# Kernel optimization log

Measured on AMD Instinct MI355X. Metric: run time of the kernel, lower is better.

The kernel has to match this reference:

```python
import jax, jax.numpy as jnp
import numpy as np

B, Himg, Wimg, C, NH = 16, 64, 64, 256, 8
HD = C // NH  # 32
N = Himg * Wimg  # 4096


def _rotations(h, w, hd):
    # RMT/RAVLT 2D axial RoPE: head_dim split into two halves (rows, cols),
    # each half holds k_max = hd//4 complex frequencies.
    k_max = hd // 4
    theta = 1.0 / (10000.0 ** (np.arange(k_max) / k_max))
    ang_h = np.arange(h)[:, None] * theta  # (h, k_max)
    ang_w = np.arange(w)[:, None] * theta  # (w, k_max)
    ang = np.concatenate([
        np.broadcast_to(ang_h[:, None, :], (h, w, k_max)),
        np.broadcast_to(ang_w[None, :, :], (h, w, k_max)),
    ], axis=-1)  # (h, w, hd//2)
    return jnp.asarray(np.cos(ang), jnp.float32), jnp.asarray(np.sin(ang), jnp.float32)

COS, SIN = _rotations(Himg, Wimg, HD)


def _rope(x):
    # x: (b, nh, H, W, hd); complex rotation of (even, odd) channel pairs
    xr, xi = x[..., 0::2], x[..., 1::2]
    out_r = xr * COS - xi * SIN
    out_i = xr * SIN + xi * COS
    return jnp.stack([out_r, out_i], axis=-1).reshape(x.shape)


def setup_inputs() -> dict:
    key = jax.random.key(0)
    ks = jax.random.split(key, 5)
    return {
        "x": jax.random.normal(ks[0], (B, N, C), jnp.float32),
        "w_qkvo": jax.random.normal(ks[1], (C, 4 * C), jnp.float32) * 0.02,
        "b_qkvo": jnp.zeros((4 * C,), jnp.float32),
        "lepe_w": jax.random.normal(ks[2], (C, 1, 5, 5), jnp.float32) * 0.02,
        "lepe_b": jnp.zeros((C,), jnp.float32),
        "w_proj": jax.random.normal(ks[3], (C, C), jnp.float32) * 0.02,
        "b_proj": jnp.zeros((C,), jnp.float32),
    }


def reference(x, w_qkvo, b_qkvo, lepe_w, lepe_b, w_proj, b_proj):
    b, n, c = x.shape
    scale = HD ** -0.5
    qkvo = x @ w_qkvo + b_qkvo  # (b, n, 4c)
    q, k, v, o = (qkvo[..., i * c:(i + 1) * c] for i in range(4))
    # LePE: depthwise 5x5 conv on v viewed as an image
    v_img = v.reshape(b, Himg, Wimg, c).transpose(0, 3, 1, 2)  # NCHW
    lepe = jax.lax.conv_general_dilated(
        v_img, lepe_w, window_strides=(1, 1), padding=[(2, 2), (2, 2)],
        dimension_numbers=("NCHW", "OIHW", "NCHW"), feature_group_count=c,
    ) + lepe_b[None, :, None, None]
    # ELU+1 feature map
    q = jax.nn.elu(q) + 1.0
    k = jax.nn.elu(k) + 1.0
    q = q.reshape(b, n, NH, HD).transpose(0, 2, 1, 3)  # (b, nh, n, hd)
    k = k.reshape(b, n, NH, HD).transpose(0, 2, 1, 3)
    v = v.reshape(b, n, NH, HD).transpose(0, 2, 1, 3)
    # efficiency reweighting of keys
    q_mean = q.mean(axis=-2, keepdims=True)  # (b, nh, 1, hd)
    eff = jax.nn.softmax(scale * jnp.einsum("bhod,bhnd->bhon", q_mean, k), axis=-1)
    k = k * eff.transpose(0, 1, 3, 2) * n  # (b, nh, n, hd)
    # RoPE on q and reweighted k
    q_rope = _rope(q.reshape(b, NH, Himg, Wimg, HD)).reshape(b, NH, n, HD)
    k_rope = _rope(k.reshape(b, NH, Himg, Wimg, HD)).reshape(b, NH, n, HD)
    # normalizer from non-rope q and mean of reweighted k
    z = 1.0 / (jnp.einsum("bhnd,bhod->bhno", q, k.mean(axis=-2, keepdims=True)) + 1e-6)
    # linear attention: kv accumulation then q @ kv (scale n^-1 split as n^-0.5 each)
    inv_sqrt_n = n ** -0.5
    kv = jnp.einsum("bhnd,bhne->bhde", k_rope * inv_sqrt_n, v * inv_sqrt_n)  # (b, nh, hd, hd)
    out = jnp.einsum("bhnd,bhde->bhne", q_rope, kv) * z
    out = out.transpose(0, 2, 1, 3).reshape(b, n, c)
    out = out + lepe.transpose(0, 2, 3, 1).reshape(b, n, c)
    out = out * o  # gate
    return out @ w_proj + b_proj
```

## Files before the change

### kernel.cpp

```cpp
#include <hip/hip_runtime.h>
#include <math.h>

constexpr int B   = 16;
constexpr int IH  = 64;
constexpr int IW  = 64;
constexpr int C   = 256;
constexpr int NH  = 8;
constexpr int HD  = 32;
constexpr int N   = IH * IW;
constexpr int C4  = 4 * C;
constexpr int KVP_STRIDE = 1060;

using f16x8 = __attribute__((ext_vector_type(8))) _Float16;
using f32x4 = __attribute__((ext_vector_type(4))) float;

__global__ void k_prologue(const float* __restrict__ w_qkvo,
                           const float* __restrict__ w_proj,
                           float* __restrict__ cosT, float* __restrict__ sinT,
                           _Float16* __restrict__ wqh, _Float16* __restrict__ wql,
                           _Float16* __restrict__ wph, _Float16* __restrict__ wpl) {
  int bid = blockIdx.x;
  int tid = threadIdx.x;
  if (bid < 256) {
    int t = bid * 256 + tid;
    int j = t & 15, pix = t >> 4;
    int y = pix >> 6, x = pix & 63;
    int jj = j & 7;
    double theta = pow(10000.0, -(double)jj / 8.0);
    double pos = (j < 8) ? (double)y : (double)x;
    double ang = pos * theta;
    cosT[t] = (float)cos(ang);
    sinT[t] = (float)sin(ang);
  } else if (bid < 256 + C4) {
    int n = bid - 256;
    float v = w_qkvo[(size_t)tid * C4 + n];
    _Float16 h = (_Float16)v;
    wqh[(size_t)n * 256 + tid] = h;
    wql[(size_t)n * 256 + tid] = (_Float16)(v - (float)h);
  } else {
    int n = bid - 256 - C4;
    float v = w_proj[(size_t)tid * C + n];
    _Float16 h = (_Float16)v;
    wph[(size_t)n * 256 + tid] = h;
    wpl[(size_t)n * 256 + tid] = (_Float16)(v - (float)h);
  }
}

__global__ __launch_bounds__(256) void k_gemm_split(
    const float* __restrict__ A, int lda,
    const _Float16* __restrict__ BhT, const _Float16* __restrict__ BlT,
    const float* __restrict__ bias, float* __restrict__ Cm, int ldc,
    int nelu, float* __restrict__ qpart) {
  __shared__ _Float16 lds[4 * 5120];
  _Float16* AhL = lds;
  _Float16* AlL = lds + 5120;
  _Float16* BhL = lds + 10240;
  _Float16* BlL = lds + 15360;
  int t = threadIdx.x;
  int m0 = blockIdx.x * 128, n0 = blockIdx.y * 128;
  int lane = t & 63;
  int wm = t >> 7, wn = (t >> 6) & 1;
  int lr = lane & 15, lg = lane >> 4;
  int srow = t >> 1, sseg = t & 1;

  f32x4 acc[4][4] = {};

  const float* aP = &A[(size_t)(m0 + srow) * lda + sseg * 16];
  const _Float16* bhP = &BhT[(size_t)(n0 + srow) * 256 + sseg * 16];
  const _Float16* blP = &BlT[(size_t)(n0 + srow) * 256 + sseg * 16];
  float4 ar0 = *(const float4*)(aP + 0);
  float4 ar1 = *(const float4*)(aP + 4);
  float4 ar2 = *(const float4*)(aP + 8);
  float4 ar3 = *(const float4*)(aP + 12);
  f16x8 brh0 = *(const f16x8*)(bhP + 0);
  f16x8 brh1 = *(const f16x8*)(bhP + 8);
  f16x8 brl0 = *(const f16x8*)(blP + 0);
  f16x8 brl1 = *(const f16x8*)(blP + 8);

  for (int kc = 0; kc < 256; kc += 32) {
    {
      float av[16] = {ar0.x, ar0.y, ar0.z, ar0.w, ar1.x, ar1.y, ar1.z, ar1.w,
                      ar2.x, ar2.y, ar2.z, ar2.w, ar3.x, ar3.y, ar3.z, ar3.w};
      f16x8 h0, h1, l0, l1;
#pragma unroll
      for (int j = 0; j < 8; ++j) {
        _Float16 h = (_Float16)av[j];
        h0[j] = h; l0[j] = (_Float16)(av[j] - (float)h);
        _Float16 h2 = (_Float16)av[j + 8];
        h1[j] = h2; l1[j] = (_Float16)(av[j + 8] - (float)h2);
      }
      int d = srow * 40 + sseg * 16;
      *(f16x8*)&AhL[d] = h0; *(f16x8*)&AhL[d + 8] = h1;
      *(f16x8*)&AlL[d] = l0; *(f16x8*)&AlL[d + 8] = l1;
      *(f16x8*)&BhL[d] = brh0; *(f16x8*)&BhL[d + 8] = brh1;
      *(f16x8*)&BlL[d] = brl0; *(f16x8*)&BlL[d + 8] = brl1;
    }
    __syncthreads();

    if (kc + 32 < 256) {
      const float* aN = aP + kc + 32;
      const _Float16* bhN = bhP + kc + 32;
      const _Float16* blN = blP + kc + 32;
      ar0 = *(const float4*)(aN + 0);
      ar1 = *(const float4*)(aN + 4);
      ar2 = *(const float4*)(aN + 8);
      ar3 = *(const float4*)(aN + 12);
      brh0 = *(const f16x8*)(bhN + 0);
      brh1 = *(const f16x8*)(bhN + 8);
      brl0 = *(const f16x8*)(blN + 0);
      brl1 = *(const f16x8*)(blN + 8);
    }

    f16x8 ah[4], al[4];
#pragma unroll
    for (int mi = 0; mi < 4; ++mi) {
      int ar = (wm * 64 + mi * 16 + lr) * 40 + lg * 8;
      ah[mi] = *(const f16x8*)&AhL[ar];
      al[mi] = *(const f16x8*)&AlL[ar];
    }
#pragma unroll
    for (int ni = 0; ni < 4; ++ni) {
      int br = (wn * 64 + ni * 16 + lr) * 40 + lg * 8;
      f16x8 bh = *(const f16x8*)&BhL[br];
      f16x8 bl = *(const f16x8*)&BlL[br];
#pragma unroll
      for (int mi = 0; mi < 4; ++mi) {
        acc[mi][ni] = __builtin_amdgcn_mfma_f32_16x16x32_f16(ah[mi], bh, acc[mi][ni], 0, 0, 0);
        acc[mi][ni] = __builtin_amdgcn_mfma_f32_16x16x32_f16(al[mi], bh, acc[mi][ni], 0, 0, 0);
        acc[mi][ni] = __builtin_amdgcn_mfma_f32_16x16x32_f16(ah[mi], bl, acc[mi][ni], 0, 0, 0);
      }
    }
    __syncthreads();
  }

  float* Cl = reinterpret_cast<float*>(lds);
  int ri2 = t >> 3, c0 = (t & 7) << 4;
  bool doq = (qpart != nullptr) && (n0 < 256);
  float qs[16] = {};
#pragma unroll
  for (int mi = 0; mi < 4; ++mi) {
#pragma unroll
    for (int ni = 0; ni < 4; ++ni) {
      int col = wn * 64 + ni * 16 + lr;
#pragma unroll
      for (int r = 0; r < 4; ++r)
        Cl[(wm * 16 + lg * 4 + r) * 132 + col] = acc[mi][ni][r];
    }
    __syncthreads();
    int grow = m0 + (ri2 >> 4) * 64 + mi * 16 + (ri2 & 15);
#pragma unroll
    for (int j = 0; j < 4; ++j) {
      int col = n0 + c0 + j * 4;
      float4 v = *(const float4*)&Cl[ri2 * 132 + c0 + j * 4];
      float4 bb = *(const float4*)&bias[col];
      v.x += bb.x; v.y += bb.y; v.z += bb.z; v.w += bb.w;
      if (col < nelu) {
        v.x = (v.x > 0.f) ? v.x + 1.f : expf(v.x);
        v.y = (v.y > 0.f) ? v.y + 1.f : expf(v.y);
        v.z = (v.z > 0.f) ? v.z + 1.f : expf(v.z);
        v.w = (v.w > 0.f) ? v.w + 1.f : expf(v.w);
      }
      if (doq) {
        qs[j * 4 + 0] += v.x; qs[j * 4 + 1] += v.y;
        qs[j * 4 + 2] += v.z; qs[j * 4 + 3] += v.w;
      }
      *(float4*)&Cm[(size_t)grow * ldc + col] = v;
    }
    __syncthreads();
  }
  if (doq) {
#pragma unroll
    for (int j = 0; j < 4; ++j) {
      float4 w4 = {qs[j*4+0], qs[j*4+1], qs[j*4+2], qs[j*4+3]};
      *(float4*)&Cl[ri2 * 132 + c0 + j * 4] = w4;
    }
    __syncthreads();
    if (t < 128) {
      float ssum = 0.f;
#pragma unroll
      for (int rr = 0; rr < 32; ++rr) ssum += Cl[rr * 132 + t];
      int b_local = m0 >> 12, rowblk = (m0 >> 7) & 31;
      qpart[(size_t)(b_local * 32 + rowblk) * 256 + n0 + t] = ssum;
    }
  }
}

__global__ __launch_bounds__(256) void k_kvflash_lepe(
    const float* __restrict__ qkvo, const float* __restrict__ qpart,
    const float* __restrict__ cosT, const float* __restrict__ sinT,
    float* __restrict__ kvp,
    const float* __restrict__ lepe_w, const float* __restrict__ lepe_b,
    float* __restrict__ lepe_out, int b0, int kvN) {
  __shared__ float qm[32];
  __shared__ float sL[512];
  __shared__ float red[256];
  __shared__ float ktG[4][32][36];
  __shared__ float vtG[4][32][36];
  int bid = blockIdx.x;
  int t = threadIdx.x;

  if (bid >= kvN) {
    int blk = bid - kvN;
    int b = blk >> 8, rem = blk & 255;
    int y = rem >> 2, x0 = (rem & 3) << 4;
    int c = t;
    float w[25];
#pragma unroll
    for (int i = 0; i < 25; ++i) w[i] = lepe_w[c * 25 + i];
    float bias = lepe_b[c];
    float acc[16];
#pragma unroll
    for (int p = 0; p < 16; ++p) acc[p] = bias;
#pragma unroll
    for (int dy = 0; dy < 5; ++dy) {
      int yy = y + dy - 2;
      if (yy < 0 || yy >= IH) continue;
      size_t rowb = (size_t)(b * N + (yy << 6)) * C4 + 512 + c;
#pragma unroll
      for (int dx = 0; dx < 5; ++dx) {
        float wv = w[dy * 5 + dx];
#pragma unroll
        for (int p = 0; p < 16; ++p) {
          int xx = x0 + p + dx - 2;
          if (xx < 0 || xx >= IW) continue;
          acc[p] = fmaf(qkvo[rowb + (size_t)xx * C4], wv, acc[p]);
        }
      }
    }
#pragma unroll
    for (int p = 0; p < 16; ++p)
      lepe_out[(size_t)((b0 + b) * N + (y << 6) + x0 + p) * C + c] = acc[p];
    return;
  }

  int bh = bid >> 3, chunk = bid & 7;
  int b = bh >> 3, h = bh & 7;
  int nbase = chunk << 9;

  if (t < 32) {
    float s = 0.f;
#pragma unroll
    for (int rb = 0; rb < 32; ++rb)
      s += qpart[(size_t)(b * 32 + rb) * 256 + (h << 5) + t];
    qm[t] = s * (1.0f / N) * 0.1767766952966369f;
  }
  __syncthreads();

  float qmr[32];
#pragma unroll
  for (int i = 0; i < 32; ++i) qmr[i] = qm[i];
  float mx = -3.4e38f;
#pragma unroll
  for (int i = 0; i < 2; ++i) {
    int n = nbase + t + i * 256;
    const float* kp = &qkvo[(size_t)(b * N + n) * C4 + 256 + (h << 5)];
    float dot = 0.f;
#pragma unroll
    for (int j = 0; j < 8; ++j) {
      float4 k4 = *(const float4*)(kp + (j << 2));
      dot += k4.x * qmr[j*4] + k4.y * qmr[j*4+1] + k4.z * qmr[j*4+2] + k4.w * qmr[j*4+3];
    }
    sL[t + i * 256] = dot;
    mx = fmaxf(mx, dot);
  }
  red[t] = mx; __syncthreads();
  for (int off = 128; off > 0; off >>= 1) {
    if (t < off) red[t] = fmaxf(red[t], red[t + off]);
    __syncthreads();
  }
  float mx_c = red[0];
  __syncthreads();
  float psum = expf(sL[t] - mx_c) + expf(sL[t + 256] - mx_c);
  red[t] = psum; __syncthreads();
  for (int off = 128; off > 0; off >>= 1) {
    if (t < off) red[t] += red[t + off];
    __syncthreads();
  }
  float sum_c = red[0];

  int sg = t >> 6;
  int lane = t & 63;
  int d0 = (lane >> 3) << 2;
  int e0 = (lane & 7) << 2;
  int srow_l = (t >> 1) & 31;
  int sdh = t & 1;
  float acc[4][4] = {};
  float km16[16] = {};

  for (int s = 0; s < 4; ++s) {
    int nloc = sg * 128 + s * 32 + srow_l;
    int n = nbase + nloc;
    const float* kp = &qkvo[(size_t)(b * N + n) * C4 + 256 + (h << 5) + sdh * 16];
    const float* vp = kp + 256;
    float ef = expf(sL[nloc] - mx_c);
    float kl[16], vl[16];
#pragma unroll
    for (int j4 = 0; j4 < 4; ++j4) {
      float4 k4 = *(const float4*)(kp + (j4 << 2));
      float4 v4 = *(const float4*)(vp + (j4 << 2));
      k4.x *= ef; k4.y *= ef; k4.z *= ef; k4.w *= ef;
      km16[j4*4+0] += k4.x; km16[j4*4+1] += k4.y;
      km16[j4*4+2] += k4.z; km16[j4*4+3] += k4.w;
      kl[j4*4+0] = k4.x; kl[j4*4+1] = k4.y; kl[j4*4+2] = k4.z; kl[j4*4+3] = k4.w;
      vl[j4*4+0] = v4.x; vl[j4*4+1] = v4.y; vl[j4*4+2] = v4.z; vl[j4*4+3] = v4.w;
    }
#pragma unroll
    for (int p = 0; p < 8; ++p) {
      float cc = cosT[(n << 4) + sdh * 8 + p];
      float sn = sinT[(n << 4) + sdh * 8 + p];
      float kr = kl[2*p], ki = kl[2*p+1];
      kl[2*p]   = kr * cc - ki * sn;
      kl[2*p+1] = kr * sn + ki * cc;
    }
#pragma unroll
    for (int j4 = 0; j4 < 4; ++j4) {
      float4 kw = {kl[j4*4+0], kl[j4*4+1], kl[j4*4+2], kl[j4*4+3]};
      float4 vw = {vl[j4*4+0], vl[j4*4+1], vl[j4*4+2], vl[j4*4+3]};
      *(float4*)&ktG[sg][srow_l][sdh*16 + (j4 << 2)] = kw;
      *(float4*)&vtG[sg][srow_l][sdh*16 + (j4 << 2)] = vw;
    }
    __syncthreads();
    __builtin_amdgcn_s_setprio(1);
#pragma unroll
    for (int nn = 0; nn < 32; ++nn) {
      float4 k4 = *(const float4*)&ktG[sg][nn][d0];
      float4 v4 = *(const float4*)&vtG[sg][nn][e0];
      float kv_[4] = {k4.x, k4.y, k4.z, k4.w};
      float vv_[4] = {v4.x, v4.y, v4.z, v4.w};
#pragma unroll
      for (int i = 0; i < 4; ++i)
#pragma unroll
        for (int j = 0; j < 4; ++j)
          acc[i][j] = fmaf(kv_[i], vv_[j], acc[i][j]);
    }
    __builtin_amdgcn_s_setprio(0);
    __syncthreads();
  }

  float* mrg = &ktG[0][0][0];
#pragma unroll
  for (int i = 0; i < 4; ++i)
#pragma unroll
    for (int j = 0; j < 4; ++j)
      mrg[sg * 1024 + (d0 + i) * 32 + (e0 + j)] = acc[i][j];
  __syncthreads();
  size_t o = (size_t)(bh * 8 + chunk) * KVP_STRIDE;
  {
    int idx = t << 2;
    float4 r;
    r.x = mrg[idx+0] + mrg[1024+idx+0] + mrg[2048+idx+0] + mrg[3072+idx+0];
    r.y = mrg[idx+1] + mrg[1024+idx+1] + mrg[2048+idx+1] + mrg[3072+idx+1];
    r.z = mrg[idx+2] + mrg[1024+idx+2] + mrg[2048+idx+2] + mrg[3072+idx+2];
    r.w = mrg[idx+3] + mrg[1024+idx+3] + mrg[2048+idx+3] + mrg[3072+idx+3];
    kvp[o + idx + 0] = r.x; kvp[o + idx + 1] = r.y;
    kvp[o + idx + 2] = r.z; kvp[o + idx + 3] = r.w;
  }
  float* kmb = &vtG[0][0][0];
#pragma unroll
  for (int j = 0; j < 16; ++j) kmb[t * 16 + j] = km16[j];
  __syncthreads();
  if (t < 32) {
    int dh = t >> 4, dj = t & 15;
    float ssum = 0.f;
    for (int r = 0; r < 128; ++r) ssum += kmb[((r << 1) + dh) * 16 + dj];
    kvp[o + 1024 + t] = ssum;
  }
  if (t == 0) {
    kvp[o + 1056] = mx_c;
    kvp[o + 1057] = sum_c;
  }
}

__global__ __launch_bounds__(256) void k_out_combine(
    float* __restrict__ qkvo, const float* __restrict__ kvp,
    const float* __restrict__ cosT, const float* __restrict__ sinT,
    const float* __restrict__ lepe, int b0) {
  __shared__ float kvs[1024];
  __shared__ float kms[32];
  __shared__ float fcs[8];
  int bh = blockIdx.x, chunk = blockIdx.y;
  int b = bh >> 3, h = bh & 7;
  int t = threadIdx.x;
  if (t == 0) {
    float mxs[8], sums[8];
    float mx = -3.4e38f;
#pragma unroll
    for (int c = 0; c < 8; ++c) {
      size_t o = (size_t)(bh * 8 + c) * KVP_STRIDE;
      mxs[c] = kvp[o + 1056];
      sums[c] = kvp[o + 1057];
      mx = fmaxf(mx, mxs[c]);
    }
    float T = 0.f;
#pragma unroll
    for (int c = 0; c < 8; ++c) T += sums[c] * expf(mxs[c] - mx);
    float invT = 1.0f / T;
#pragma unroll
    for (int c = 0; c < 8; ++c) fcs[c] = expf(mxs[c] - mx) * invT;
  }
  __syncthreads();
  {
    int idx = t << 2;
    size_t o0 = (size_t)(bh * 8) * KVP_STRIDE + idx;
    float4 r = {0.f, 0.f, 0.f, 0.f};
#pragma unroll
    for (int c = 0; c < 8; ++c) {
      float4 p = *(const float4*)&kvp[o0 + (size_t)c * KVP_STRIDE];
      float f = fcs[c];
      r.x += p.x * f; r.y += p.y * f; r.z += p.z * f; r.w += p.w * f;
    }
    *(float4*)&kvs[idx] = r;
    if (t < 32) {
      float s = 0.f;
#pragma unroll
      for (int c = 0; c < 8; ++c)
        s += kvp[(size_t)(bh * 8 + c) * KVP_STRIDE + 1024 + t] * fcs[c];
      kms[t] = s;
    }
  }
  __syncthreads();
  int n = (chunk << 8) + t;
  size_t rowbase = (size_t)(b * N + n) * C4;
  float q[32];
#pragma unroll
  for (int i = 0; i < 8; ++i) {
    float4 q4 = *reinterpret_cast<const float4*>(&qkvo[rowbase + (h << 5) + (i << 2)]);
    q[i * 4 + 0] = q4.x; q[i * 4 + 1] = q4.y; q[i * 4 + 2] = q4.z; q[i * 4 + 3] = q4.w;
  }
  float dot = 0.f;
#pragma unroll
  for (int dd = 0; dd < 32; ++dd) dot += q[dd] * kms[dd];
  float zv = 1.0f / (dot + 1e-6f);
  const float* cp = &cosT[n << 4];
  const float* sp = &sinT[n << 4];
#pragma unroll
  for (int j = 0; j < 16; ++j) {
    float cc = cp[j], ss = sp[j];
    float qr = q[2 * j], qi = q[2 * j + 1];
    q[2 * j]     = qr * cc - qi * ss;
    q[2 * j + 1] = qr * ss + qi * cc;
  }
  size_t oc = (size_t)((b0 + b) * N + n) * C + (h << 5);
#pragma unroll
  for (int e4 = 0; e4 < 8; ++e4) {
    float ax = 0, ay = 0, az = 0, aw = 0;
#pragma unroll
    for (int dd = 0; dd < 32; ++dd) {
      float4 kv4 = *reinterpret_cast<const float4*>(&kvs[(dd << 5) + (e4 << 2)]);
      float qd = q[dd];
      ax = fmaf(qd, kv4.x, ax); ay = fmaf(qd, kv4.y, ay);
      az = fmaf(qd, kv4.z, az); aw = fmaf(qd, kv4.w, aw);
    }
    float4 lp = *reinterpret_cast<const float4*>(&lepe[oc + (e4 << 2)]);
    float4 ov = *reinterpret_cast<const float4*>(
        &qkvo[rowbase + 768 + (h << 5) + (e4 << 2)]);
    float4 r;
    r.x = (ax * zv + lp.x) * ov.x;
    r.y = (ay * zv + lp.y) * ov.y;
    r.z = (az * zv + lp.z) * ov.z;
    r.w = (aw * zv + lp.w) * ov.w;
    *reinterpret_cast<float4*>(&qkvo[rowbase + (h << 5) + (e4 << 2)]) = r;
  }
}

static inline size_t ws_bytes_needed(int bpp) {
  size_t pn = (size_t)bpp * N;
  size_t f32c = pn * C4
              + (size_t)bpp * 32 * 256
              + (size_t)bpp * NH * 8 * KVP_STRIDE
              + (size_t)N * 16 * 2;
  size_t f16c = (size_t)C * C4 * 2
              + (size_t)C * C * 2;
  return f32c * 4 + f16c * 2;
}

extern "C" void kernel_launch(void* const* d_in, const int* in_sizes, int n_in,
                              void* d_out, int out_size, void* d_ws, size_t ws_size,
                              hipStream_t stream) {
  const float* x      = (const float*)d_in[0];
  const float* w_qkvo = (const float*)d_in[1];
  const float* b_qkvo = (const float*)d_in[2];
  const float* lepe_w = (const float*)d_in[3];
  const float* lepe_b = (const float*)d_in[4];
  const float* w_proj = (const float*)d_in[5];
  const float* b_proj = (const float*)d_in[6];
  float* out = (float*)d_out;
  float* ws  = (float*)d_ws;

  int bpp = 2;
  if (ws_bytes_needed(16) <= ws_size) bpp = 16;
  else if (ws_bytes_needed(8) <= ws_size) bpp = 8;
  else if (ws_bytes_needed(4) <= ws_size) bpp = 4;

  size_t pn = (size_t)bpp * N;
  int nbh = bpp * NH;
  float* qkvo  = ws;
  float* qpart = qkvo  + pn * C4;
  float* kvp   = qpart + (size_t)bpp * 32 * 256;
  float* cosT  = kvp   + (size_t)nbh * 8 * KVP_STRIDE;
  float* sinT  = cosT  + (size_t)N * 16;
  _Float16* wqh = (_Float16*)(sinT + (size_t)N * 16);
  _Float16* wql = wqh + (size_t)C * C4;
  _Float16* wph = wql + (size_t)C * C4;
  _Float16* wpl = wph + (size_t)C * C;

  k_prologue<<<256 + C4 + C, 256, 0, stream>>>(w_qkvo, w_proj, cosT, sinT,
                                               wqh, wql, wph, wpl);

  for (int b0 = 0; b0 < B; b0 += bpp) {
    k_gemm_split<<<dim3(pn / 128, C4 / 128), 256, 0, stream>>>(
        x + (size_t)b0 * N * C, C, wqh, wql, b_qkvo, qkvo, C4, 512, qpart);
    int kvN = nbh * 8;
    k_kvflash_lepe<<<kvN + bpp * 256, 256, 0, stream>>>(
        qkvo, qpart, cosT, sinT, kvp, lepe_w, lepe_b, out, b0, kvN);
    k_out_combine<<<dim3(nbh, 16), 256, 0, stream>>>(qkvo, kvp, cosT, sinT, out, b0);
    k_gemm_split<<<dim3(pn / 128, C / 128), 256, 0, stream>>>(
        qkvo, C4, wph, wpl, b_proj, out + (size_t)b0 * N * C, C, 0, nullptr);
  }
}
```

Before: 507.5 us.

## Pad GEMM LDS row stride and process two pixels per thread in combine

```diff
diff --git a/kernel.cpp b/kernel.cpp
--- a/kernel.cpp
+++ b/kernel.cpp
@@ -10,6 +10,8 @@
 constexpr int N   = IH * IW;
 constexpr int C4  = 4 * C;
 constexpr int KVP_STRIDE = 1060;
+constexpr int LSTR = 44;
+constexpr int LBUF = 128 * LSTR;
 
 using f16x8 = __attribute__((ext_vector_type(8))) _Float16;
 using f32x4 = __attribute__((ext_vector_type(4))) float;
@@ -51,11 +53,11 @@
     const _Float16* __restrict__ BhT, const _Float16* __restrict__ BlT,
     const float* __restrict__ bias, float* __restrict__ Cm, int ldc,
     int nelu, float* __restrict__ qpart) {
-  __shared__ _Float16 lds[4 * 5120];
+  __shared__ _Float16 lds[4 * LBUF];
   _Float16* AhL = lds;
-  _Float16* AlL = lds + 5120;
-  _Float16* BhL = lds + 10240;
-  _Float16* BlL = lds + 15360;
+  _Float16* AlL = lds + LBUF;
+  _Float16* BhL = lds + 2 * LBUF;
+  _Float16* BlL = lds + 3 * LBUF;
   int t = threadIdx.x;
   int m0 = blockIdx.x * 128, n0 = blockIdx.y * 128;
   int lane = t & 63;
@@ -89,7 +91,7 @@
         _Float16 h2 = (_Float16)av[j + 8];
         h1[j] = h2; l1[j] = (_Float16)(av[j + 8] - (float)h2);
       }
-      int d = srow * 40 + sseg * 16;
+      int d = srow * LSTR + sseg * 16;
       *(f16x8*)&AhL[d] = h0; *(f16x8*)&AhL[d + 8] = h1;
       *(f16x8*)&AlL[d] = l0; *(f16x8*)&AlL[d + 8] = l1;
       *(f16x8*)&BhL[d] = brh0; *(f16x8*)&BhL[d + 8] = brh1;
@@ -114,13 +116,13 @@
     f16x8 ah[4], al[4];
 #pragma unroll
     for (int mi = 0; mi < 4; ++mi) {
-      int ar = (wm * 64 + mi * 16 + lr) * 40 + lg * 8;
+      int ar = (wm * 64 + mi * 16 + lr) * LSTR + lg * 8;
       ah[mi] = *(const f16x8*)&AhL[ar];
       al[mi] = *(const f16x8*)&AlL[ar];
     }
 #pragma unroll
     for (int ni = 0; ni < 4; ++ni) {
-      int br = (wn * 64 + ni * 16 + lr) * 40 + lg * 8;
+      int br = (wn * 64 + ni * 16 + lr) * LSTR + lg * 8;
       f16x8 bh = *(const f16x8*)&BhL[br];
       f16x8 bl = *(const f16x8*)&BlL[br];
 #pragma unroll
@@ -419,47 +421,68 @@
     }
   }
   __syncthreads();
-  int n = (chunk << 8) + t;
-  size_t rowbase = (size_t)(b * N + n) * C4;
-  float q[32];
+  int n1 = (chunk << 8) + t;
+  int n2 = n1 + 2048;
+  size_t rb1 = (size_t)(b * N + n1) * C4;
+  size_t rb2 = (size_t)(b * N + n2) * C4;
+  float q1[32], q2[32];
 #pragma unroll
   for (int i = 0; i < 8; ++i) {
-    float4 q4 = *reinterpret_cast<const float4*>(&qkvo[rowbase + (h << 5) + (i << 2)]);
-    q[i * 4 + 0] = q4.x; q[i * 4 + 1] = q4.y; q[i * 4 + 2] = q4.z; q[i * 4 + 3] = q4.w;
-  }
-  float dot = 0.f;
-#pragma unroll
-  for (int dd = 0; dd < 32; ++dd) dot += q[dd] * kms[dd];
-  float zv = 1.0f / (dot + 1e-6f);
-  const float* cp = &cosT[n << 4];
-  const float* sp = &sinT[n << 4];
+    float4 a4 = *(const float4*)&qkvo[rb1 + (h << 5) + (i << 2)];
+    float4 b4 = *(const float4*)&qkvo[rb2 + (h << 5) + (i << 2)];
+    q1[i*4+0] = a4.x; q1[i*4+1] = a4.y; q1[i*4+2] = a4.z; q1[i*4+3] = a4.w;
+    q2[i*4+0] = b4.x; q2[i*4+1] = b4.y; q2[i*4+2] = b4.z; q2[i*4+3] = b4.w;
+  }
+  float dot1 = 0.f, dot2 = 0.f;
+#pragma unroll
+  for (int dd = 0; dd < 32; ++dd) {
+    dot1 += q1[dd] * kms[dd];
+    dot2 += q2[dd] * kms[dd];
+  }
+  float zv1 = 1.0f / (dot1 + 1e-6f);
+  float zv2 = 1.0f / (dot2 + 1e-6f);
 #pragma unroll
   for (int j = 0; j < 16; ++j) {
-    float cc = cp[j], ss = sp[j];
-    float qr = q[2 * j], qi = q[2 * j + 1];
-    q[2 * j]     = qr * cc - qi * ss;
-    q[2 * j + 1] = qr * ss + qi * cc;
-  }
-  size_t oc = (size_t)((b0 + b) * N + n) * C + (h << 5);
+    float c1 = cosT[(n1 << 4) + j], s1 = sinT[(n1 << 4) + j];
+    float qr = q1[2*j], qi = q1[2*j+1];
+    q1[2*j]   = qr * c1 - qi * s1;
+    q1[2*j+1] = qr * s1 + qi * c1;
+    float c2 = cosT[(n2 << 4) + j], s2 = sinT[(n2 << 4) + j];
+    float kr = q2[2*j], ki = q2[2*j+1];
+    q2[2*j]   = kr * c2 - ki * s2;
+    q2[2*j+1] = kr * s2 + ki * c2;
+  }
+  size_t oc1 = (size_t)((b0 + b) * N + n1) * C + (h << 5);
+  size_t oc2 = (size_t)((b0 + b) * N + n2) * C + (h << 5);
 #pragma unroll
   for (int e4 = 0; e4 < 8; ++e4) {
-    float ax = 0, ay = 0, az = 0, aw = 0;
+    float a1x = 0, a1y = 0, a1z = 0, a1w = 0;
+    float a2x = 0, a2y = 0, a2z = 0, a2w = 0;
 #pragma unroll
     for (int dd = 0; dd < 32; ++dd) {
-      float4 kv4 = *reinterpret_cast<const float4*>(&kvs[(dd << 5) + (e4 << 2)]);
-      float qd = q[dd];
-      ax = fmaf(qd, kv4.x, ax); ay = fmaf(qd, kv4.y, ay);
-      az = fmaf(qd, kv4.z, az); aw = fmaf(qd, kv4.w, aw);
-    }
-    float4 lp = *reinterpret_cast<const float4*>(&lepe[oc + (e4 << 2)]);
-    float4 ov = *reinterpret_cast<const float4*>(
-        &qkvo[rowbase + 768 + (h << 5) + (e4 << 2)]);
-    float4 r;
-    r.x = (ax * zv + lp.x) * ov.x;
-    r.y = (ay * zv + lp.y) * ov.y;
-    r.z = (az * zv + lp.z) * ov.z;
-    r.w = (aw * zv + lp.w) * ov.w;
-    *reinterpret_cast<float4*>(&qkvo[rowbase + (h << 5) + (e4 << 2)]) = r;
+      float4 kv4 = *(const float4*)&kvs[(dd << 5) + (e4 << 2)];
+      float qa = q1[dd], qb = q2[dd];
+      a1x = fmaf(qa, kv4.x, a1x); a1y = fmaf(qa, kv4.y, a1y);
+      a1z = fmaf(qa, kv4.z, a1z); a1w = fmaf(qa, kv4.w, a1w);
+      a2x = fmaf(qb, kv4.x, a2x); a2y = fmaf(qb, kv4.y, a2y);
+      a2z = fmaf(qb, kv4.z, a2z); a2w = fmaf(qb, kv4.w, a2w);
+    }
+    float4 lp1 = *(const float4*)&lepe[oc1 + (e4 << 2)];
+    float4 ov1 = *(const float4*)&qkvo[rb1 + 768 + (h << 5) + (e4 << 2)];
+    float4 r1;
+    r1.x = (a1x * zv1 + lp1.x) * ov1.x;
+    r1.y = (a1y * zv1 + lp1.y) * ov1.y;
+    r1.z = (a1z * zv1 + lp1.z) * ov1.z;
+    r1.w = (a1w * zv1 + lp1.w) * ov1.w;
+    *(float4*)&qkvo[rb1 + (h << 5) + (e4 << 2)] = r1;
+    float4 lp2 = *(const float4*)&lepe[oc2 + (e4 << 2)];
+    float4 ov2 = *(const float4*)&qkvo[rb2 + 768 + (h << 5) + (e4 << 2)];
+    float4 r2;
+    r2.x = (a2x * zv2 + lp2.x) * ov2.x;
+    r2.y = (a2y * zv2 + lp2.y) * ov2.y;
+    r2.z = (a2z * zv2 + lp2.z) * ov2.z;
+    r2.w = (a2w * zv2 + lp2.w) * ov2.w;
+    *(float4*)&qkvo[rb2 + (h << 5) + (e4 << 2)] = r2;
   }
 }
 
@@ -513,7 +536,7 @@
     int kvN = nbh * 8;
     k_kvflash_lepe<<<kvN + bpp * 256, 256, 0, stream>>>(
         qkvo, qpart, cosT, sinT, kvp, lepe_w, lepe_b, out, b0, kvN);
-    k_out_combine<<<dim3(nbh, 16), 256, 0, stream>>>(qkvo, kvp, cosT, sinT, out, b0);
+    k_out_combine<<<dim3(nbh, 8), 256, 0, stream>>>(qkvo, kvp, cosT, sinT, out, b0);
     k_gemm_split<<<dim3(pn / 128, C / 128), 256, 0, stream>>>(
         qkvo, C4, wph, wpl, b_proj, out + (size_t)b0 * N * C, C, 0, nullptr);
   }
```

Result: slower. 709.4 us (+39.8%).
